# Performance work log

Hardware: AMD Instinct MI355X
Metric: run time of the kernel (lower is better)

Reference implementation:

```python
import jax, jax.numpy as jnp
import numpy as np

B, N, D, H = 4, 4096, 128, 4
LN_EPS = 1e-5
SIG_EPS = 1e-6


def setup_inputs() -> dict:
    key = jax.random.key(0)
    k1, k2 = jax.random.split(key)
    x = jax.random.normal(k1, (B, N, D), dtype=jnp.float32)
    log_sigmas = jnp.zeros((H, 1, 1), dtype=jnp.float32)
    proj_w = jax.random.normal(k2, (D, D), dtype=jnp.float32) * (1.0 / np.sqrt(D))
    proj_b = jnp.zeros((D,), dtype=jnp.float32)
    ln_gamma = jnp.ones((D,), dtype=jnp.float32)
    ln_beta = jnp.zeros((D,), dtype=jnp.float32)
    return {"x": x, "log_sigmas": log_sigmas, "proj_w": proj_w,
            "proj_b": proj_b, "ln_gamma": ln_gamma, "ln_beta": ln_beta}


def reference(x, log_sigmas, proj_w, proj_b, ln_gamma, ln_beta):
    # x: [b, n, d]
    # squared pairwise Euclidean distances: [b, n, n]
    x2 = jnp.sum(x * x, axis=-1)
    gram = jnp.einsum('bnd,bmd->bnm', x, x)
    dist_sq = jnp.maximum(x2[:, :, None] + x2[:, None, :] - 2.0 * gram, 0.0)
    # per-head RBF adjacency, averaged over heads: [b, n, n]
    sigmas = jnp.exp(log_sigmas).reshape(-1)  # [h]
    denom = 2.0 * sigmas ** 2 + SIG_EPS       # [h]
    adjs = jnp.exp(-dist_sq[:, None, :, :] / denom[None, :, None, None])  # [b,h,n,n]
    adj_final = adjs.mean(axis=1)              # [b, n, n]
    # diffusion + projection
    out = jnp.einsum('bnm,bmd->bnd', adj_final, x)
    out = out @ proj_w.T + proj_b
    # ELU + residual + LayerNorm
    y = jax.nn.elu(out) + x
    mu = jnp.mean(y, axis=-1, keepdims=True)
    var = jnp.mean((y - mu) ** 2, axis=-1, keepdims=True)
    return (y - mu) / jnp.sqrt(var + LN_EPS) * ln_gamma + ln_beta
```

## Files before the change

kernel.cpp:

```cpp
#include <hip/hip_runtime.h>
#include <hip/hip_bf16.h>

#define BB 4
#define NN 4096
#define DD 128

typedef __attribute__((ext_vector_type(8))) short bf16x8;
typedef __attribute__((ext_vector_type(16))) float f32x16;

__device__ __forceinline__ unsigned short f2bf(float f) {
    unsigned u = __float_as_uint(f);
    return (unsigned short)((u + 0x7FFFu + ((u >> 16) & 1u)) >> 16);
}
__device__ __forceinline__ float bf2f(unsigned short s) {
    return __uint_as_float((unsigned)s << 16);
}
__device__ __forceinline__ unsigned pk2(float a, float b) {
    return (unsigned)f2bf(a) | ((unsigned)f2bf(b) << 16);
}


__global__ __launch_bounds__(512) void prep_kernel(const float* __restrict__ x,
        const float* __restrict__ W, short* __restrict__ xbF,
        short* __restrict__ vF, short* __restrict__ wbF, float* __restrict__ x2) {
    if (blockIdx.x >= 256) {
        int t = (blockIdx.x - 256) * 512 + threadIdx.x;
        int j = t >> 5, cq = t & 31;
        float4 v = *(const float4*)(W + j * 128 + cq * 4);
        uint2 pk; pk.x = pk2(v.x, v.y); pk.y = pk2(v.z, v.w);
        *(uint2*)(wbF + (j >> 5) * 4096 + (cq >> 1) * 256 + (j & 31) * 8 + (cq & 1) * 4) = pk;
        return;
    }
    __shared__ short Ls[64 * 136];
    int tid = threadIdx.x;
    int r = tid >> 3, cq = tid & 7;
    size_t rowg = (size_t)blockIdx.x * 64 + r;
    const float* xp = x + rowg * DD + cq * 16;
    short tmp[16];
    float s = 0.f;
    #pragma unroll
    for (int i = 0; i < 4; ++i) {
        float4 v = ((const float4*)xp)[i];
        unsigned short b0 = f2bf(v.x), b1 = f2bf(v.y), b2 = f2bf(v.z), b3 = f2bf(v.w);
        tmp[i*4+0] = (short)b0; tmp[i*4+1] = (short)b1;
        tmp[i*4+2] = (short)b2; tmp[i*4+3] = (short)b3;
        float f0 = bf2f(b0), f1 = bf2f(b1), f2 = bf2f(b2), f3 = bf2f(b3);
        s += f0*f0 + f1*f1 + f2*f2 + f3*f3;
    }
    #pragma unroll
    for (int c = 0; c < 2; ++c) {
        uint4 v = ((uint4*)tmp)[c];
        *(uint4*)(xbF + (rowg >> 5) * 4096 + (size_t)(cq * 2 + c) * 256 + (rowg & 31) * 8) = v;
        *(uint4*)(&Ls[r * 136 + cq * 16 + c * 8]) = v;
    }
    s += __shfl_xor(s, 1); s += __shfl_xor(s, 2); s += __shfl_xor(s, 4);
    if (cq == 0) x2[rowg] = s;
    __syncthreads();
    int d = tid & 127, q = tid >> 7;
    short arr[16];
    #pragma unroll
    for (int i = 0; i < 16; ++i) arr[i] = Ls[(q * 16 + i) * 136 + d];
    int blk = blockIdx.x, b = blk >> 6;
    int g0 = (blk & 63) * 8 + q * 2;
    size_t base = (size_t)b * 524288 + (size_t)(d >> 5) * 131072 + (size_t)(d & 31) * 8;
    *(uint4*)(vF + base + (size_t)g0 * 256)       = ((uint4*)arr)[0];
    *(uint4*)(vF + base + (size_t)(g0 + 1) * 256) = ((uint4*)arr)[1];
}

__global__ __launch_bounds__(512, 2) void attn_kernel(
        const short* __restrict__ xbF, const short* __restrict__ vF,
        const float* __restrict__ x2, const short* __restrict__ wbF,
        const float* __restrict__ log_sigmas, const float* __restrict__ pb,
        const float* __restrict__ x, const float* __restrict__ gamma,
        const float* __restrict__ beta, float* __restrict__ out) {
    __shared__ char smem[34816] __attribute__((aligned(128)));
    float* O_lds = (float*)smem;

    int tid = threadIdx.x, lane = tid & 63, w = tid >> 6;
    int l5 = lane & 31, hi = lane >> 5;

    int bid = (blockIdx.x & 7) * 32 + (blockIdx.x >> 3);
    int b = bid >> 6, n0 = (bid & 63) * 64;

    const short* xf_b = xbF + (size_t)b * 524288;
    const short* vf_b = vF + (size_t)b * 524288;
    const float* x2b = x2 + (size_t)b * NN;

    #pragma unroll
    for (int i = 0; i < 17; ++i) O_lds[tid + 512 * i] = 0.f;

    float invd[4];
    #pragma unroll
    for (int h = 0; h < 4; ++h) {
        float sg = __expf(log_sigmas[h]);
        invd[h] = 1.0f / (2.0f * sg * sg + 1e-6f);
    }
    bool same = (invd[0] == invd[1]) && (invd[1] == invd[2]) && (invd[2] == invd[3]);
    float c0 = -invd[0];
    float invd_min = fminf(fminf(invd[0], invd[1]), fminf(invd[2], invd[3]));
    float thr = 30.0f / invd_min;

    bf16x8 qa[8], qb[8];
    {
        const short* qp = xf_b + (size_t)(n0 >> 5) * 4096;
        #pragma unroll
        for (int ck = 0; ck < 8; ++ck) {
            qa[ck] = *(const bf16x8*)(qp + (2 * ck + hi) * 256 + l5 * 8);
            qb[ck] = *(const bf16x8*)(qp + 4096 + (2 * ck + hi) * 256 + l5 * 8);
        }
    }
    float x2nA = x2b[n0 + l5], x2nB = x2b[n0 + 32 + l5];

    __syncthreads();

    bf16x8 kc[8];
    {
        const short* kp = xf_b + (size_t)w * 4096;
        #pragma unroll
        for (int ck = 0; ck < 8; ++ck)
            kc[ck] = *(const bf16x8*)(kp + (2 * ck + hi) * 256 + l5 * 8);
    }

    for (int s = w; s < 128; s += 8) {
        bf16x8 kn[8];
        if (s + 8 < 128) {
            const short* kp = xf_b + (size_t)(s + 8) * 4096;
            #pragma unroll
            for (int ck = 0; ck < 8; ++ck)
                kn[ck] = *(const bf16x8*)(kp + (2 * ck + hi) * 256 + l5 * 8);
        }
        float4 t0 = *(const float4*)(x2b + s * 32 + 4 * hi);
        float4 t1 = *(const float4*)(x2b + s * 32 + 8 + 4 * hi);
        float4 t2 = *(const float4*)(x2b + s * 32 + 16 + 4 * hi);
        float4 t3 = *(const float4*)(x2b + s * 32 + 24 + 4 * hi);
        float xmv[16];
        xmv[0]=t0.x; xmv[1]=t0.y; xmv[2]=t0.z; xmv[3]=t0.w;
        xmv[4]=t1.x; xmv[5]=t1.y; xmv[6]=t1.z; xmv[7]=t1.w;
        xmv[8]=t2.x; xmv[9]=t2.y; xmv[10]=t2.z; xmv[11]=t2.w;
        xmv[12]=t3.x; xmv[13]=t3.y; xmv[14]=t3.z; xmv[15]=t3.w;

        f32x16 SA, SB;
        #pragma unroll
        for (int i = 0; i < 16; ++i) { SA[i] = 0.f; SB[i] = 0.f; }
        #pragma unroll
        for (int ck = 0; ck < 8; ++ck) {
            SA = __builtin_amdgcn_mfma_f32_32x32x16_bf16(kc[ck], qa[ck], SA, 0, 0, 0);
            SB = __builtin_amdgcn_mfma_f32_32x32x16_bf16(kc[ck], qb[ck], SB, 0, 0, 0);
        }
        float dvA[16], dvB[16];
        #pragma unroll
        for (int i = 0; i < 16; ++i) {
            dvA[i] = x2nA + xmv[i] - 2.0f * SA[i];
            dvB[i] = x2nB + xmv[i] - 2.0f * SB[i];
        }
        float pmin = dvA[0];
        #pragma unroll
        for (int i = 1; i < 16; ++i) pmin = fminf(pmin, dvA[i]);
        #pragma unroll
        for (int i = 0; i < 16; ++i) pmin = fminf(pmin, dvB[i]);

        if (!__all(pmin > thr)) {
            float wA[16], wB[16];
            #pragma unroll
            for (int i = 0; i < 16; ++i) {
                float cA = fmaxf(dvA[i], 0.f), cB = fmaxf(dvB[i], 0.f);
                if (same) {
                    wA[i] = __expf(cA * c0);
                    wB[i] = __expf(cB * c0);
                } else {
                    wA[i] = 0.25f * (__expf(-cA * invd[0]) + __expf(-cA * invd[1]) +
                                     __expf(-cA * invd[2]) + __expf(-cA * invd[3]));
                    wB[i] = 0.25f * (__expf(-cB * invd[0]) + __expf(-cB * invd[1]) +
                                     __expf(-cB * invd[2]) + __expf(-cB * invd[3]));
                }
            }
            unsigned pAlo[4], pAhi[4], pBlo[4], pBhi[4];
            #pragma unroll
            for (int G = 0; G < 4; ++G) {
                pAlo[G] = pk2(wA[4*G+0], wA[4*G+1]);
                pAhi[G] = pk2(wA[4*G+2], wA[4*G+3]);
                pBlo[G] = pk2(wB[4*G+0], wB[4*G+1]);
                pBhi[G] = pk2(wB[4*G+2], wB[4*G+3]);
            }
            uint4 fA[2], fB[2];
            #pragma unroll
            for (int ks = 0; ks < 2; ++ks) {
                unsigned oAl = hi ? pAlo[2*ks+1] : pAlo[2*ks];
                unsigned oAh = hi ? pAhi[2*ks+1] : pAhi[2*ks];
                unsigned sAl = hi ? pAlo[2*ks]   : pAlo[2*ks+1];
                unsigned sAh = hi ? pAhi[2*ks]   : pAhi[2*ks+1];
                unsigned rAl = __shfl_xor(sAl, 32);
                unsigned rAh = __shfl_xor(sAh, 32);
                fA[ks].x = hi ? rAl : oAl;  fA[ks].y = hi ? rAh : oAh;
                fA[ks].z = hi ? oAl : rAl;  fA[ks].w = hi ? oAh : rAh;
                unsigned oBl = hi ? pBlo[2*ks+1] : pBlo[2*ks];
                unsigned oBh = hi ? pBhi[2*ks+1] : pBhi[2*ks];
                unsigned sBl = hi ? pBlo[2*ks]   : pBlo[2*ks+1];
                unsigned sBh = hi ? pBhi[2*ks]   : pBhi[2*ks+1];
                unsigned rBl = __shfl_xor(sBl, 32);
                unsigned rBh = __shfl_xor(sBh, 32);
                fB[ks].x = hi ? rBl : oBl;  fB[ks].y = hi ? rBh : oBh;
                fB[ks].z = hi ? oBl : rBl;  fB[ks].w = hi ? oBh : rBh;
            }
            bf16x8 wfA0 = *(bf16x8*)&fA[0], wfA1 = *(bf16x8*)&fA[1];
            bf16x8 wfB0 = *(bf16x8*)&fB[0], wfB1 = *(bf16x8*)&fB[1];
            #pragma unroll
            for (int db = 0; db < 4; ++db) {
                const short* vp = vf_b + db * 131072 + (size_t)s * 4 * 256;
                bf16x8 v0 = *(const bf16x8*)(vp + (size_t)(0 + hi) * 256 + l5 * 8);
                bf16x8 v1 = *(const bf16x8*)(vp + (size_t)(2 + hi) * 256 + l5 * 8);
                f32x16 DA, DB;
                #pragma unroll
                for (int i = 0; i < 16; ++i) { DA[i] = 0.f; DB[i] = 0.f; }
                DA = __builtin_amdgcn_mfma_f32_32x32x16_bf16(v0, wfA0, DA, 0, 0, 0);
                DA = __builtin_amdgcn_mfma_f32_32x32x16_bf16(v1, wfA1, DA, 0, 0, 0);
                DB = __builtin_amdgcn_mfma_f32_32x32x16_bf16(v0, wfB0, DB, 0, 0, 0);
                DB = __builtin_amdgcn_mfma_f32_32x32x16_bf16(v1, wfB1, DB, 0, 0, 0);
                #pragma unroll
                for (int i = 0; i < 16; ++i) {
                    int droff = (i & 3) + 8 * (i >> 2) + 4 * hi;
                    atomicAdd(&O_lds[(db * 32 + droff) * 68 + l5], DA[i]);
                    atomicAdd(&O_lds[(db * 32 + droff) * 68 + 32 + l5], DB[i]);
                }
            }
        }
        if (s + 8 < 128) {
            #pragma unroll
            for (int ck = 0; ck < 8; ++ck) kc[ck] = kn[ck];
        }
    }

    __syncthreads();

    int jq = w & 3, nh2 = w >> 2;
    bf16x8 af[8];
    #pragma unroll
    for (int ck = 0; ck < 8; ++ck) {
        unsigned u0, u1, u2, u3;
        {
            int dbase = ck * 16 + hi * 8;
            int nn = nh2 * 32 + l5;
            u0 = pk2(O_lds[(dbase + 0) * 68 + nn], O_lds[(dbase + 1) * 68 + nn]);
            u1 = pk2(O_lds[(dbase + 2) * 68 + nn], O_lds[(dbase + 3) * 68 + nn]);
            u2 = pk2(O_lds[(dbase + 4) * 68 + nn], O_lds[(dbase + 5) * 68 + nn]);
            u3 = pk2(O_lds[(dbase + 6) * 68 + nn], O_lds[(dbase + 7) * 68 + nn]);
        }
        uint4 uu; uu.x = u0; uu.y = u1; uu.z = u2; uu.w = u3;
        af[ck] = *(bf16x8*)&uu;
    }
    f32x16 P;
    #pragma unroll
    for (int i = 0; i < 16; ++i) P[i] = 0.f;
    {
        const short* wp = wbF + jq * 4096;
        #pragma unroll
        for (int ck = 0; ck < 8; ++ck) {
            bf16x8 bf = *(const bf16x8*)(wp + (2 * ck + hi) * 256 + l5 * 8);
            P = __builtin_amdgcn_mfma_f32_32x32x16_bf16(af[ck], bf, P, 0, 0, 0);
        }
    }
    float pbj = pb[jq * 32 + l5];
    __syncthreads();
    float* Plds = (float*)smem;
    #pragma unroll
    for (int i = 0; i < 16; ++i) {
        int roff = (i & 3) + 8 * (i >> 2) + 4 * hi;
        Plds[(nh2 * 32 + roff) * 132 + jq * 32 + l5] = P[i] + pbj;
    }
    __syncthreads();

    {
        int row = tid >> 3, part = tid & 7;
        const float* xr = x + ((size_t)b * NN + n0 + row) * DD + part * 16;
        float y[16];
        float sum = 0.f, ss = 0.f;
        #pragma unroll
        for (int c = 0; c < 4; ++c) {
            float4 pv = *(const float4*)(Plds + row * 132 + part * 16 + c * 4);
            float4 xv = *(const float4*)(xr + c * 4);
            #pragma unroll
            for (int k = 0; k < 4; ++k) {
                float p = ((const float*)&pv)[k];
                float e = (p > 0.f ? p : __expf(p) - 1.f) + ((const float*)&xv)[k];
                y[c * 4 + k] = e;
                sum += e; ss += e * e;
            }
        }
        sum += __shfl_xor(sum, 1); ss += __shfl_xor(ss, 1);
        sum += __shfl_xor(sum, 2); ss += __shfl_xor(ss, 2);
        sum += __shfl_xor(sum, 4); ss += __shfl_xor(ss, 4);
        float mu = sum * 0.0078125f;
        float var = fmaxf(ss * 0.0078125f - mu * mu, 0.f);
        float inv = rsqrtf(var + 1e-5f);
        float* op = out + ((size_t)b * NN + n0 + row) * DD + part * 16;
        #pragma unroll
        for (int c = 0; c < 4; ++c) {
            float4 gv = *(const float4*)(gamma + part * 16 + c * 4);
            float4 bv = *(const float4*)(beta + part * 16 + c * 4);
            float4 o;
            ((float*)&o)[0] = (y[c*4+0] - mu) * inv * ((const float*)&gv)[0] + ((const float*)&bv)[0];
            ((float*)&o)[1] = (y[c*4+1] - mu) * inv * ((const float*)&gv)[1] + ((const float*)&bv)[1];
            ((float*)&o)[2] = (y[c*4+2] - mu) * inv * ((const float*)&gv)[2] + ((const float*)&bv)[2];
            ((float*)&o)[3] = (y[c*4+3] - mu) * inv * ((const float*)&gv)[3] + ((const float*)&bv)[3];
            *(float4*)(op + c * 4) = o;
        }
    }
}

extern "C" void kernel_launch(void* const* d_in, const int* in_sizes, int n_in,
                              void* d_out, int out_size, void* d_ws, size_t ws_size,
                              hipStream_t stream) {
    const float* x  = (const float*)d_in[0];
    const float* ls = (const float*)d_in[1];
    const float* pw = (const float*)d_in[2];
    const float* pb = (const float*)d_in[3];
    const float* g  = (const float*)d_in[4];
    const float* be = (const float*)d_in[5];
    float* out = (float*)d_out;

    char* ws = (char*)d_ws;
    short* xbF = (short*)ws;
    short* vF  = (short*)(ws + (size_t)4 * 1024 * 1024);
    float* x2  = (float*)(ws + (size_t)8 * 1024 * 1024);
    short* wbF = (short*)(ws + (size_t)8 * 1024 * 1024 + 65536);

    prep_kernel<<<dim3(264), dim3(512), 0, stream>>>(x, pw, xbF, vF, wbF, x2);
    attn_kernel<<<dim3(BB * NN / 64), dim3(512), 0, stream>>>(
        xbF, vF, x2, wbF, ls, pb, x, g, be, out);
}
```

Baseline: 57.87 us.

## Split query halves across waves with 1024-thread blocks and per-half skip test

Doubles the attention block to 1024 threads so each wave owns one 32-row query half instead of both halves. This halves per-wave accumulator and query registers and makes the far-distance skip test per half, so more tiles can be skipped. It also drops the software prefetch of the next key tile, leaves the projection to only 8 waves, and moves the LayerNorm to 16 threads per row. The aggressive launch bound of 1024 threads with 4 blocks may force a tight VGPR cap and cause spills, and the deeper LDS atomic contention on O_lds adds cost.

```diff
diff --git a/kernel.cpp b/kernel.cpp
--- a/kernel.cpp
+++ b/kernel.cpp
@@ -67,7 +67,7 @@
     *(uint4*)(vF + base + (size_t)(g0 + 1) * 256) = ((uint4*)arr)[1];
 }
 
-__global__ __launch_bounds__(512, 2) void attn_kernel(
+__global__ __launch_bounds__(1024, 4) void attn_kernel(
         const short* __restrict__ xbF, const short* __restrict__ vF,
         const float* __restrict__ x2, const short* __restrict__ wbF,
         const float* __restrict__ log_sigmas, const float* __restrict__ pb,
@@ -78,6 +78,7 @@
 
     int tid = threadIdx.x, lane = tid & 63, w = tid >> 6;
     int l5 = lane & 31, hi = lane >> 5;
+    int nh = w & 1, sgrp = w >> 1;
 
     int bid = (blockIdx.x & 7) * 32 + (blockIdx.x >> 3);
     int b = bid >> 6, n0 = (bid & 63) * 64;
@@ -87,7 +88,8 @@
     const float* x2b = x2 + (size_t)b * NN;
 
     #pragma unroll
-    for (int i = 0; i < 17; ++i) O_lds[tid + 512 * i] = 0.f;
+    for (int i = 0; i < 8; ++i) O_lds[tid + 1024 * i] = 0.f;
+    if (tid < 512) O_lds[8192 + tid] = 0.f;
 
     float invd[4];
     #pragma unroll
@@ -100,35 +102,25 @@
     float invd_min = fminf(fminf(invd[0], invd[1]), fminf(invd[2], invd[3]));
     float thr = 30.0f / invd_min;
 
-    bf16x8 qa[8], qb[8];
+    bf16x8 qa[8];
     {
-        const short* qp = xf_b + (size_t)(n0 >> 5) * 4096;
-        #pragma unroll
-        for (int ck = 0; ck < 8; ++ck) {
+        const short* qp = xf_b + (size_t)((n0 >> 5) + nh) * 4096;
+        #pragma unroll
+        for (int ck = 0; ck < 8; ++ck)
             qa[ck] = *(const bf16x8*)(qp + (2 * ck + hi) * 256 + l5 * 8);
-            qb[ck] = *(const bf16x8*)(qp + 4096 + (2 * ck + hi) * 256 + l5 * 8);
-        }
-    }
-    float x2nA = x2b[n0 + l5], x2nB = x2b[n0 + 32 + l5];
-
-    __syncthreads();
-
-    bf16x8 kc[8];
-    {
-        const short* kp = xf_b + (size_t)w * 4096;
+    }
+    float x2n = x2b[n0 + nh * 32 + l5];
+    float limit = x2n - thr;
+
+    __syncthreads();
+
+    for (int t = 0; t < 16; ++t) {
+        int s = sgrp + t * 8;
+        const short* kp = xf_b + (size_t)s * 4096;
+        bf16x8 kc[8];
         #pragma unroll
         for (int ck = 0; ck < 8; ++ck)
             kc[ck] = *(const bf16x8*)(kp + (2 * ck + hi) * 256 + l5 * 8);
-    }
-
-    for (int s = w; s < 128; s += 8) {
-        bf16x8 kn[8];
-        if (s + 8 < 128) {
-            const short* kp = xf_b + (size_t)(s + 8) * 4096;
-            #pragma unroll
-            for (int ck = 0; ck < 8; ++ck)
-                kn[ck] = *(const bf16x8*)(kp + (2 * ck + hi) * 256 + l5 * 8);
-        }
         float4 t0 = *(const float4*)(x2b + s * 32 + 4 * hi);
         float4 t1 = *(const float4*)(x2b + s * 32 + 8 + 4 * hi);
         float4 t2 = *(const float4*)(x2b + s * 32 + 16 + 4 * hi);
@@ -139,50 +131,36 @@
         xmv[8]=t2.x; xmv[9]=t2.y; xmv[10]=t2.z; xmv[11]=t2.w;
         xmv[12]=t3.x; xmv[13]=t3.y; xmv[14]=t3.z; xmv[15]=t3.w;
 
-        f32x16 SA, SB;
-        #pragma unroll
-        for (int i = 0; i < 16; ++i) { SA[i] = 0.f; SB[i] = 0.f; }
-        #pragma unroll
-        for (int ck = 0; ck < 8; ++ck) {
+        f32x16 SA;
+        #pragma unroll
+        for (int i = 0; i < 16; ++i) SA[i] = 0.f;
+        #pragma unroll
+        for (int ck = 0; ck < 8; ++ck)
             SA = __builtin_amdgcn_mfma_f32_32x32x16_bf16(kc[ck], qa[ck], SA, 0, 0, 0);
-            SB = __builtin_amdgcn_mfma_f32_32x32x16_bf16(kc[ck], qb[ck], SB, 0, 0, 0);
-        }
-        float dvA[16], dvB[16];
-        #pragma unroll
-        for (int i = 0; i < 16; ++i) {
-            dvA[i] = x2nA + xmv[i] - 2.0f * SA[i];
-            dvB[i] = x2nB + xmv[i] - 2.0f * SB[i];
-        }
-        float pmin = dvA[0];
-        #pragma unroll
-        for (int i = 1; i < 16; ++i) pmin = fminf(pmin, dvA[i]);
-        #pragma unroll
-        for (int i = 0; i < 16; ++i) pmin = fminf(pmin, dvB[i]);
-
-        if (!__all(pmin > thr)) {
-            float wA[16], wB[16];
+
+        float e[16];
+        #pragma unroll
+        for (int i = 0; i < 16; ++i) e[i] = fmaf(2.0f, SA[i], -xmv[i]);
+        float lmax = e[0];
+        #pragma unroll
+        for (int i = 1; i < 16; ++i) lmax = fmaxf(lmax, e[i]);
+
+        if (__any(lmax >= limit)) {
+            float wA[16];
             #pragma unroll
             for (int i = 0; i < 16; ++i) {
-                float cA = fmaxf(dvA[i], 0.f), cB = fmaxf(dvB[i], 0.f);
-                if (same) {
-                    wA[i] = __expf(cA * c0);
-                    wB[i] = __expf(cB * c0);
-                } else {
-                    wA[i] = 0.25f * (__expf(-cA * invd[0]) + __expf(-cA * invd[1]) +
-                                     __expf(-cA * invd[2]) + __expf(-cA * invd[3]));
-                    wB[i] = 0.25f * (__expf(-cB * invd[0]) + __expf(-cB * invd[1]) +
-                                     __expf(-cB * invd[2]) + __expf(-cB * invd[3]));
-                }
-            }
-            unsigned pAlo[4], pAhi[4], pBlo[4], pBhi[4];
+                float cA = fmaxf(x2n - e[i], 0.f);
+                if (same) wA[i] = __expf(cA * c0);
+                else wA[i] = 0.25f * (__expf(-cA * invd[0]) + __expf(-cA * invd[1]) +
+                                      __expf(-cA * invd[2]) + __expf(-cA * invd[3]));
+            }
+            unsigned pAlo[4], pAhi[4];
             #pragma unroll
             for (int G = 0; G < 4; ++G) {
                 pAlo[G] = pk2(wA[4*G+0], wA[4*G+1]);
                 pAhi[G] = pk2(wA[4*G+2], wA[4*G+3]);
-                pBlo[G] = pk2(wB[4*G+0], wB[4*G+1]);
-                pBhi[G] = pk2(wB[4*G+2], wB[4*G+3]);
-            }
-            uint4 fA[2], fB[2];
+            }
+            uint4 fA[2];
             #pragma unroll
             for (int ks = 0; ks < 2; ++ks) {
                 unsigned oAl = hi ? pAlo[2*ks+1] : pAlo[2*ks];
@@ -193,110 +171,95 @@
                 unsigned rAh = __shfl_xor(sAh, 32);
                 fA[ks].x = hi ? rAl : oAl;  fA[ks].y = hi ? rAh : oAh;
                 fA[ks].z = hi ? oAl : rAl;  fA[ks].w = hi ? oAh : rAh;
-                unsigned oBl = hi ? pBlo[2*ks+1] : pBlo[2*ks];
-                unsigned oBh = hi ? pBhi[2*ks+1] : pBhi[2*ks];
-                unsigned sBl = hi ? pBlo[2*ks]   : pBlo[2*ks+1];
-                unsigned sBh = hi ? pBhi[2*ks]   : pBhi[2*ks+1];
-                unsigned rBl = __shfl_xor(sBl, 32);
-                unsigned rBh = __shfl_xor(sBh, 32);
-                fB[ks].x = hi ? rBl : oBl;  fB[ks].y = hi ? rBh : oBh;
-                fB[ks].z = hi ? oBl : rBl;  fB[ks].w = hi ? oBh : rBh;
             }
             bf16x8 wfA0 = *(bf16x8*)&fA[0], wfA1 = *(bf16x8*)&fA[1];
-            bf16x8 wfB0 = *(bf16x8*)&fB[0], wfB1 = *(bf16x8*)&fB[1];
             #pragma unroll
             for (int db = 0; db < 4; ++db) {
                 const short* vp = vf_b + db * 131072 + (size_t)s * 4 * 256;
                 bf16x8 v0 = *(const bf16x8*)(vp + (size_t)(0 + hi) * 256 + l5 * 8);
                 bf16x8 v1 = *(const bf16x8*)(vp + (size_t)(2 + hi) * 256 + l5 * 8);
-                f32x16 DA, DB;
+                f32x16 DA;
                 #pragma unroll
-                for (int i = 0; i < 16; ++i) { DA[i] = 0.f; DB[i] = 0.f; }
+                for (int i = 0; i < 16; ++i) DA[i] = 0.f;
                 DA = __builtin_amdgcn_mfma_f32_32x32x16_bf16(v0, wfA0, DA, 0, 0, 0);
                 DA = __builtin_amdgcn_mfma_f32_32x32x16_bf16(v1, wfA1, DA, 0, 0, 0);
-                DB = __builtin_amdgcn_mfma_f32_32x32x16_bf16(v0, wfB0, DB, 0, 0, 0);
-                DB = __builtin_amdgcn_mfma_f32_32x32x16_bf16(v1, wfB1, DB, 0, 0, 0);
                 #pragma unroll
                 for (int i = 0; i < 16; ++i) {
                     int droff = (i & 3) + 8 * (i >> 2) + 4 * hi;
-                    atomicAdd(&O_lds[(db * 32 + droff) * 68 + l5], DA[i]);
-                    atomicAdd(&O_lds[(db * 32 + droff) * 68 + 32 + l5], DB[i]);
+                    atomicAdd(&O_lds[(db * 32 + droff) * 68 + nh * 32 + l5], DA[i]);
                 }
             }
         }
-        if (s + 8 < 128) {
-            #pragma unroll
-            for (int ck = 0; ck < 8; ++ck) kc[ck] = kn[ck];
-        }
-    }
-
-    __syncthreads();
-
-    int jq = w & 3, nh2 = w >> 2;
-    bf16x8 af[8];
-    #pragma unroll
-    for (int ck = 0; ck < 8; ++ck) {
-        unsigned u0, u1, u2, u3;
-        {
+    }
+
+    __syncthreads();
+
+    if (w < 8) {
+        int jq = w & 3, nh2 = w >> 2;
+        bf16x8 af[8];
+        #pragma unroll
+        for (int ck = 0; ck < 8; ++ck) {
             int dbase = ck * 16 + hi * 8;
             int nn = nh2 * 32 + l5;
-            u0 = pk2(O_lds[(dbase + 0) * 68 + nn], O_lds[(dbase + 1) * 68 + nn]);
-            u1 = pk2(O_lds[(dbase + 2) * 68 + nn], O_lds[(dbase + 3) * 68 + nn]);
-            u2 = pk2(O_lds[(dbase + 4) * 68 + nn], O_lds[(dbase + 5) * 68 + nn]);
-            u3 = pk2(O_lds[(dbase + 6) * 68 + nn], O_lds[(dbase + 7) * 68 + nn]);
-        }
-        uint4 uu; uu.x = u0; uu.y = u1; uu.z = u2; uu.w = u3;
-        af[ck] = *(bf16x8*)&uu;
-    }
-    f32x16 P;
-    #pragma unroll
-    for (int i = 0; i < 16; ++i) P[i] = 0.f;
-    {
+            uint4 uu;
+            uu.x = pk2(O_lds[(dbase + 0) * 68 + nn], O_lds[(dbase + 1) * 68 + nn]);
+            uu.y = pk2(O_lds[(dbase + 2) * 68 + nn], O_lds[(dbase + 3) * 68 + nn]);
+            uu.z = pk2(O_lds[(dbase + 4) * 68 + nn], O_lds[(dbase + 5) * 68 + nn]);
+            uu.w = pk2(O_lds[(dbase + 6) * 68 + nn], O_lds[(dbase + 7) * 68 + nn]);
+            af[ck] = *(bf16x8*)&uu;
+        }
+        f32x16 P;
+        #pragma unroll
+        for (int i = 0; i < 16; ++i) P[i] = 0.f;
         const short* wp = wbF + jq * 4096;
         #pragma unroll
         for (int ck = 0; ck < 8; ++ck) {
             bf16x8 bf = *(const bf16x8*)(wp + (2 * ck + hi) * 256 + l5 * 8);
             P = __builtin_amdgcn_mfma_f32_32x32x16_bf16(af[ck], bf, P, 0, 0, 0);
         }
-    }
-    float pbj = pb[jq * 32 + l5];
-    __syncthreads();
-    float* Plds = (float*)smem;
-    #pragma unroll
-    for (int i = 0; i < 16; ++i) {
-        int roff = (i & 3) + 8 * (i >> 2) + 4 * hi;
-        Plds[(nh2 * 32 + roff) * 132 + jq * 32 + l5] = P[i] + pbj;
+        float pbj = pb[jq * 32 + l5];
+        __syncthreads();
+        float* Plds = (float*)smem;
+        #pragma unroll
+        for (int i = 0; i < 16; ++i) {
+            int roff = (i & 3) + 8 * (i >> 2) + 4 * hi;
+            Plds[(nh2 * 32 + roff) * 132 + jq * 32 + l5] = P[i] + pbj;
+        }
+    } else {
+        __syncthreads();
     }
     __syncthreads();
 
     {
-        int row = tid >> 3, part = tid & 7;
-        const float* xr = x + ((size_t)b * NN + n0 + row) * DD + part * 16;
-        float y[16];
+        float* Plds = (float*)smem;
+        int row = tid >> 4, part = tid & 15;
+        const float* xr = x + ((size_t)b * NN + n0 + row) * DD + part * 8;
+        float y[8];
         float sum = 0.f, ss = 0.f;
         #pragma unroll
-        for (int c = 0; c < 4; ++c) {
-            float4 pv = *(const float4*)(Plds + row * 132 + part * 16 + c * 4);
+        for (int c = 0; c < 2; ++c) {
+            float4 pv = *(const float4*)(Plds + row * 132 + part * 8 + c * 4);
             float4 xv = *(const float4*)(xr + c * 4);
             #pragma unroll
             for (int k = 0; k < 4; ++k) {
                 float p = ((const float*)&pv)[k];
-                float e = (p > 0.f ? p : __expf(p) - 1.f) + ((const float*)&xv)[k];
-                y[c * 4 + k] = e;
-                sum += e; ss += e * e;
+                float e2 = (p > 0.f ? p : __expf(p) - 1.f) + ((const float*)&xv)[k];
+                y[c * 4 + k] = e2;
+                sum += e2; ss += e2 * e2;
             }
         }
         sum += __shfl_xor(sum, 1); ss += __shfl_xor(ss, 1);
         sum += __shfl_xor(sum, 2); ss += __shfl_xor(ss, 2);
         sum += __shfl_xor(sum, 4); ss += __shfl_xor(ss, 4);
+        sum += __shfl_xor(sum, 8); ss += __shfl_xor(ss, 8);
         float mu = sum * 0.0078125f;
         float var = fmaxf(ss * 0.0078125f - mu * mu, 0.f);
         float inv = rsqrtf(var + 1e-5f);
-        float* op = out + ((size_t)b * NN + n0 + row) * DD + part * 16;
-        #pragma unroll
-        for (int c = 0; c < 4; ++c) {
-            float4 gv = *(const float4*)(gamma + part * 16 + c * 4);
-            float4 bv = *(const float4*)(beta + part * 16 + c * 4);
+        float* op = out + ((size_t)b * NN + n0 + row) * DD + part * 8;
+        #pragma unroll
+        for (int c = 0; c < 2; ++c) {
+            float4 gv = *(const float4*)(gamma + part * 8 + c * 4);
+            float4 bv = *(const float4*)(beta + part * 8 + c * 4);
             float4 o;
             ((float*)&o)[0] = (y[c*4+0] - mu) * inv * ((const float*)&gv)[0] + ((const float*)&bv)[0];
             ((float*)&o)[1] = (y[c*4+1] - mu) * inv * ((const float*)&gv)[1] + ((const float*)&bv)[1];
@@ -325,6 +288,6 @@
     short* wbF = (short*)(ws + (size_t)8 * 1024 * 1024 + 65536);
 
     prep_kernel<<<dim3(264), dim3(512), 0, stream>>>(x, pw, xbF, vF, wbF, x2);
-    attn_kernel<<<dim3(BB * NN / 64), dim3(512), 0, stream>>>(
+    attn_kernel<<<dim3(BB * NN / 64), dim3(1024), 0, stream>>>(
         xbF, vF, x2, wbF, ls, pb, x, g, be, out);
 }
```

Result: faster. 50.18 us (-13.3%).

## Double attention block to 1024 threads and prefetch key norms

Applied to the files above, without the earlier changes.

The attention kernel now launches 1024 threads per block, so each of 16 waves processes 8 key tiles instead of 16. With one block per CU on this grid, this aims to double resident waves per CU for better latency hiding. The x2 key-norm loads are now double-buffered alongside the key fragments. The epilogue splits the projection across the first 8 waves and spreads LayerNorm over 16 lanes per row. Risks: the tighter per-thread register budget may cause spills, doubled contention on the LDS atomics, and barriers placed inside divergent branches.

```diff
diff --git a/kernel.cpp b/kernel.cpp
--- a/kernel.cpp
+++ b/kernel.cpp
@@ -67,7 +67,7 @@
     *(uint4*)(vF + base + (size_t)(g0 + 1) * 256) = ((uint4*)arr)[1];
 }
 
-__global__ __launch_bounds__(512, 2) void attn_kernel(
+__global__ __launch_bounds__(1024, 4) void attn_kernel(
         const short* __restrict__ xbF, const short* __restrict__ vF,
         const float* __restrict__ x2, const short* __restrict__ wbF,
         const float* __restrict__ log_sigmas, const float* __restrict__ pb,
@@ -87,7 +87,8 @@
     const float* x2b = x2 + (size_t)b * NN;
 
     #pragma unroll
-    for (int i = 0; i < 17; ++i) O_lds[tid + 512 * i] = 0.f;
+    for (int i = 0; i < 8; ++i) O_lds[tid + 1024 * i] = 0.f;
+    if (tid < 512) O_lds[8192 + tid] = 0.f;
 
     float invd[4];
     #pragma unroll
@@ -120,24 +121,30 @@
         for (int ck = 0; ck < 8; ++ck)
             kc[ck] = *(const bf16x8*)(kp + (2 * ck + hi) * 256 + l5 * 8);
     }
-
-    for (int s = w; s < 128; s += 8) {
+    float4 xc0 = *(const float4*)(x2b + w * 32 + 4 * hi);
+    float4 xc1 = *(const float4*)(x2b + w * 32 + 8 + 4 * hi);
+    float4 xc2 = *(const float4*)(x2b + w * 32 + 16 + 4 * hi);
+    float4 xc3 = *(const float4*)(x2b + w * 32 + 24 + 4 * hi);
+
+    for (int t = 0; t < 8; ++t) {
+        int s = w + 16 * t;
         bf16x8 kn[8];
-        if (s + 8 < 128) {
-            const short* kp = xf_b + (size_t)(s + 8) * 4096;
+        float4 xn0, xn1, xn2, xn3;
+        if (t < 7) {
+            const short* kp = xf_b + (size_t)(s + 16) * 4096;
             #pragma unroll
             for (int ck = 0; ck < 8; ++ck)
                 kn[ck] = *(const bf16x8*)(kp + (2 * ck + hi) * 256 + l5 * 8);
-        }
-        float4 t0 = *(const float4*)(x2b + s * 32 + 4 * hi);
-        float4 t1 = *(const float4*)(x2b + s * 32 + 8 + 4 * hi);
-        float4 t2 = *(const float4*)(x2b + s * 32 + 16 + 4 * hi);
-        float4 t3 = *(const float4*)(x2b + s * 32 + 24 + 4 * hi);
+            xn0 = *(const float4*)(x2b + (s + 16) * 32 + 4 * hi);
+            xn1 = *(const float4*)(x2b + (s + 16) * 32 + 8 + 4 * hi);
+            xn2 = *(const float4*)(x2b + (s + 16) * 32 + 16 + 4 * hi);
+            xn3 = *(const float4*)(x2b + (s + 16) * 32 + 24 + 4 * hi);
+        }
         float xmv[16];
-        xmv[0]=t0.x; xmv[1]=t0.y; xmv[2]=t0.z; xmv[3]=t0.w;
-        xmv[4]=t1.x; xmv[5]=t1.y; xmv[6]=t1.z; xmv[7]=t1.w;
-        xmv[8]=t2.x; xmv[9]=t2.y; xmv[10]=t2.z; xmv[11]=t2.w;
-        xmv[12]=t3.x; xmv[13]=t3.y; xmv[14]=t3.z; xmv[15]=t3.w;
+        xmv[0]=xc0.x; xmv[1]=xc0.y; xmv[2]=xc0.z; xmv[3]=xc0.w;
+        xmv[4]=xc1.x; xmv[5]=xc1.y; xmv[6]=xc1.z; xmv[7]=xc1.w;
+        xmv[8]=xc2.x; xmv[9]=xc2.y; xmv[10]=xc2.z; xmv[11]=xc2.w;
+        xmv[12]=xc3.x; xmv[13]=xc3.y; xmv[14]=xc3.z; xmv[15]=xc3.w;
 
         f32x16 SA, SB;
         #pragma unroll
@@ -224,79 +231,81 @@
                 }
             }
         }
-        if (s + 8 < 128) {
+        if (t < 7) {
             #pragma unroll
             for (int ck = 0; ck < 8; ++ck) kc[ck] = kn[ck];
+            xc0 = xn0; xc1 = xn1; xc2 = xn2; xc3 = xn3;
         }
     }
 
     __syncthreads();
 
-    int jq = w & 3, nh2 = w >> 2;
-    bf16x8 af[8];
-    #pragma unroll
-    for (int ck = 0; ck < 8; ++ck) {
-        unsigned u0, u1, u2, u3;
-        {
+    if (w < 8) {
+        int jq = w & 3, nh2 = w >> 2;
+        bf16x8 af[8];
+        #pragma unroll
+        for (int ck = 0; ck < 8; ++ck) {
             int dbase = ck * 16 + hi * 8;
             int nn = nh2 * 32 + l5;
-            u0 = pk2(O_lds[(dbase + 0) * 68 + nn], O_lds[(dbase + 1) * 68 + nn]);
-            u1 = pk2(O_lds[(dbase + 2) * 68 + nn], O_lds[(dbase + 3) * 68 + nn]);
-            u2 = pk2(O_lds[(dbase + 4) * 68 + nn], O_lds[(dbase + 5) * 68 + nn]);
-            u3 = pk2(O_lds[(dbase + 6) * 68 + nn], O_lds[(dbase + 7) * 68 + nn]);
-        }
-        uint4 uu; uu.x = u0; uu.y = u1; uu.z = u2; uu.w = u3;
-        af[ck] = *(bf16x8*)&uu;
-    }
-    f32x16 P;
-    #pragma unroll
-    for (int i = 0; i < 16; ++i) P[i] = 0.f;
-    {
+            uint4 uu;
+            uu.x = pk2(O_lds[(dbase + 0) * 68 + nn], O_lds[(dbase + 1) * 68 + nn]);
+            uu.y = pk2(O_lds[(dbase + 2) * 68 + nn], O_lds[(dbase + 3) * 68 + nn]);
+            uu.z = pk2(O_lds[(dbase + 4) * 68 + nn], O_lds[(dbase + 5) * 68 + nn]);
+            uu.w = pk2(O_lds[(dbase + 6) * 68 + nn], O_lds[(dbase + 7) * 68 + nn]);
+            af[ck] = *(bf16x8*)&uu;
+        }
+        f32x16 P;
+        #pragma unroll
+        for (int i = 0; i < 16; ++i) P[i] = 0.f;
         const short* wp = wbF + jq * 4096;
         #pragma unroll
         for (int ck = 0; ck < 8; ++ck) {
             bf16x8 bf = *(const bf16x8*)(wp + (2 * ck + hi) * 256 + l5 * 8);
             P = __builtin_amdgcn_mfma_f32_32x32x16_bf16(af[ck], bf, P, 0, 0, 0);
         }
-    }
-    float pbj = pb[jq * 32 + l5];
+        float pbj = pb[jq * 32 + l5];
+        __syncthreads();
+        float* Plds = (float*)smem;
+        #pragma unroll
+        for (int i = 0; i < 16; ++i) {
+            int roff = (i & 3) + 8 * (i >> 2) + 4 * hi;
+            Plds[(nh2 * 32 + roff) * 132 + jq * 32 + l5] = P[i] + pbj;
+        }
+    } else {
+        __syncthreads();
+    }
     __syncthreads();
-    float* Plds = (float*)smem;
-    #pragma unroll
-    for (int i = 0; i < 16; ++i) {
-        int roff = (i & 3) + 8 * (i >> 2) + 4 * hi;
-        Plds[(nh2 * 32 + roff) * 132 + jq * 32 + l5] = P[i] + pbj;
-    }
-    __syncthreads();
 
     {
-        int row = tid >> 3, part = tid & 7;
-        const float* xr = x + ((size_t)b * NN + n0 + row) * DD + part * 16;
-        float y[16];
+        float* Plds = (float*)smem;
+        int row = tid >> 4, part = tid & 15;
+        const float* xr = x + ((size_t)b * NN + n0 + row) * DD + part * 8;
+        float y[8];
         float sum = 0.f, ss = 0.f;
         #pragma unroll
-        for (int c = 0; c < 4; ++c) {
-            float4 pv = *(const float4*)(Plds + row * 132 + part * 16 + c * 4);
+        for (int c = 0; c < 2; ++c) {
+            float4 pv = *(const float4*)(Plds + row * 132 + part * 8 + c * 4);
             float4 xv = *(const float4*)(xr + c * 4);
             #pragma unroll
             for (int k = 0; k < 4; ++k) {
                 float p = ((const float*)&pv)[k];
-                float e = (p > 0.f ? p : __expf(p) - 1.f) + ((const float*)&xv)[k];
-                y[c * 4 + k] = e;
-                sum += e; ss += e * e;
+                float e2 = (p > 0.f ? p : __expf(p) - 1.f) + ((const float*)&xv)[k];
+                y[c * 4 + k] = e2;
+                sum += e2; ss += e2 * e2;
             }
         }
         sum += __shfl_xor(sum, 1); ss += __shfl_xor(ss, 1);
         sum += __shfl_xor(sum, 2); ss += __shfl_xor(ss, 2);
         sum += __shfl_xor(sum, 4); ss += __shfl_xor(ss, 4);
+        sum += __shfl_xor(sum, 8); ss += __shfl_xor(ss, 8);
         float mu = sum * 0.0078125f;
         float var = fmaxf(ss * 0.0078125f - mu * mu, 0.f);
         float inv = rsqrtf(var + 1e-5f);
-        float* op = out + ((size_t)b * NN + n0 + row) * DD + part * 16;
-        #pragma unroll
-        for (int c = 0; c < 4; ++c) {
-            float4 gv = *(const float4*)(gamma + part * 16 + c * 4);
-            float4 bv = *(const float4*)(beta + part * 16 + c * 4);
+        float* op = out + ((size_t)b * NN + n0 + row) * DD + part * 8;
+        #pragma unroll
+        for (int c = 0; c < 2; ++c) {
+            float4 gv = *(const float4*)(gamma + part * 8 + c * 4);
+            float4 bv = *(const float4*)(beta + part * 8 + c * 4);
             float4 o;
             ((float*)&o)[0] = (y[c*4+0] - mu) * inv * ((const float*)&gv)[0] + ((const float*)&bv)[0];
             ((float*)&o)[1] = (y[c*4+1] - mu) * inv * ((const float*)&gv)[1] + ((const float*)&bv)[1];
@@ -325,6 +334,6 @@
     short* wbF = (short*)(ws + (size_t)8 * 1024 * 1024 + 65536);
 
     prep_kernel<<<dim3(264), dim3(512), 0, stream>>>(x, pw, xbF, vF, wbF, x2);
-    attn_kernel<<<dim3(BB * NN / 64), dim3(512), 0, stream>>>(
+    attn_kernel<<<dim3(BB * NN / 64), dim3(1024), 0, stream>>>(
         xbF, vF, x2, wbF, ls, pb, x, g, be, out);
 }
```

Measured after the change: 215.6 us. 3.73x slower.
